# Optimization experiments

Measured on AMD Instinct MI355X. Metric: run time of the kernel, lower is better.

The kernel has to match this reference:

```python
import jax, jax.numpy as jnp
import numpy as np

T = 262144          # total packed neighbor tokens
D_IN, D_H, D_OUT = 128, 256, 128
N_SETS = 8192


def setup_inputs() -> dict:
    key = jax.random.key(0)
    k1, k2, k3, k4, k5, k6 = jax.random.split(key, 6)
    x = jax.random.normal(k1, (T, D_IN), dtype=jnp.float32)
    segment_ids = jnp.sort(jax.random.randint(k2, (T,), 0, N_SETS))
    # phi params (torch Linear: y = x @ W.T + b); store as [in, out] for einsum
    s1 = 1.0 / np.sqrt(D_IN)
    s2 = 1.0 / np.sqrt(D_H)
    W1 = jax.random.uniform(k3, (D_IN, D_H), jnp.float32, -s1, s1)
    b1 = jax.random.uniform(k4, (D_H,), jnp.float32, -s1, s1)
    W2 = jax.random.uniform(k5, (D_H, D_OUT), jnp.float32, -s2, s2)
    b2 = jax.random.uniform(k6, (D_OUT,), jnp.float32, -s2, s2)
    return {"x": x, "segment_ids": segment_ids, "num_segments": N_SETS,
            "W1": W1, "b1": b1, "W2": W2, "b2": b2}


def reference(x, segment_ids, num_segments, W1, b1, W2, b2):
    # phi: Linear -> ReLU -> Linear -> ReLU, applied to every packed token
    h = jax.nn.relu(x @ W1 + b1)            # [T, D_H]
    h = jax.nn.relu(h @ W2 + b2)            # [T, D_OUT]
    # per-set mean pool (segment mean over ragged sets)
    sums = jax.ops.segment_sum(h, segment_ids, num_segments=num_segments)  # [N, D_OUT]
    counts = jax.ops.segment_sum(jnp.ones((h.shape[0],), h.dtype), segment_ids,
                                 num_segments=num_segments)                 # [N]
    out = sums / jnp.maximum(counts, 1.0)[:, None]
    return out
```

## Files before the change

kernel.cpp:

```cpp
#include <hip/hip_runtime.h>

#define D_IN 128
#define D_H 256
#define D_OUT 128
#define N_SETS 8192
#define T_TOTAL 262144

typedef short short8 __attribute__((ext_vector_type(8)));
typedef float floatx4 __attribute__((ext_vector_type(4)));
typedef float floatx16 __attribute__((ext_vector_type(16)));
typedef unsigned int uint4v __attribute__((ext_vector_type(4)));

typedef const __attribute__((address_space(1))) unsigned int gu32;
typedef __attribute__((address_space(3))) unsigned int lu32;

union U8 { uint4v u; short8 s; };

__device__ inline unsigned short f32_bf16(float f) {
    unsigned int u = __float_as_uint(f);
    u += 0x7FFFu + ((u >> 16) & 1u);
    return (unsigned short)(u >> 16);
}

__global__ void setup_kernel(const float* __restrict__ W1, const float* __restrict__ W2,
                             unsigned short* __restrict__ W1s, unsigned short* __restrict__ W2s) {
    int t = blockIdx.x * 256 + threadIdx.x;
    int l = t & 63;
    int f = t >> 6;
    int hl = l >> 5, c31 = l & 31;
    if (f < 64) {
        int nt = f >> 3, c = f & 7;
        int k0 = c * 16 + hl * 8, n = nt * 32 + c31;
        unsigned short v[8];
#pragma unroll
        for (int j = 0; j < 8; j++) v[j] = f32_bf16(W1[(k0 + j) * D_H + n]);
#pragma unroll
        for (int j = 0; j < 8; j++) W1s[f * 512 + l * 8 + j] = v[j];
    } else {
        int g = f - 64;
        int o = g >> 4, c2 = g & 15;
        int k0 = c2 * 16 + hl * 8, n = o * 32 + c31;
        unsigned short v[8];
#pragma unroll
        for (int j = 0; j < 8; j++) v[j] = f32_bf16(W2[(k0 + j) * D_OUT + n]);
#pragma unroll
        for (int j = 0; j < 8; j++) W2s[g * 512 + l * 8 + j] = v[j];
    }
}

__global__ __launch_bounds__(768, 3) void ds_main(
    const float* __restrict__ x, const int* __restrict__ seg,
    const unsigned short* __restrict__ W1s, const float* __restrict__ b1,
    const unsigned short* __restrict__ W2s, const float* __restrict__ b2,
    float* __restrict__ out, float* __restrict__ counts)
{
    __shared__ __align__(16) unsigned short wbuf[128 * 512];
    __shared__ int ssegs[12][32];

    const int tid = threadIdx.x;
    const int wave = tid >> 6, lane = tid & 63;
    const int hl = lane >> 5, c31 = lane & 31;
    const int tok0 = blockIdx.x * 384 + wave * 32;
    const bool active = (tok0 < T_TOTAL);

    if (wave < 8) {
#pragma unroll
        for (int i = 0; i < 8; i++) {
            __builtin_amdgcn_global_load_lds((gu32*)(W1s + i * 4096 + tid * 8),
                                             (lu32*)(wbuf + i * 4096 + tid * 8), 16, 0, 0);
            __builtin_amdgcn_global_load_lds((gu32*)(W2s + i * 4096 + tid * 8),
                                             (lu32*)(wbuf + 32768 + i * 4096 + tid * 8), 16, 0, 0);
        }
    }

    int* sseg = ssegs[wave];

    short8 xfa[8];
    if (active) {
        if (lane < 32) sseg[lane] = seg[tok0 + lane];
        const float* xp = x + (size_t)(tok0 + c31) * D_IN + hl * 8;
#pragma unroll
        for (int c = 0; c < 8; c++) {
            float4 v0 = *(const float4*)(xp + c * 16);
            float4 v1 = *(const float4*)(xp + c * 16 + 4);
            unsigned int p0, p1, p2, p3;
            asm("v_cvt_pk_bf16_f32 %0, %1, %2" : "=v"(p0) : "v"(v0.x), "v"(v0.y));
            asm("v_cvt_pk_bf16_f32 %0, %1, %2" : "=v"(p1) : "v"(v0.z), "v"(v0.w));
            asm("v_cvt_pk_bf16_f32 %0, %1, %2" : "=v"(p2) : "v"(v1.x), "v"(v1.y));
            asm("v_cvt_pk_bf16_f32 %0, %1, %2" : "=v"(p3) : "v"(v1.z), "v"(v1.w));
            U8 u; u.u = (uint4v){p0, p1, p2, p3};
            xfa[c] = u.s;
        }
    }

    floatx16 acc2[4];
#pragma unroll
    for (int o = 0; o < 4; o++)
#pragma unroll
        for (int i = 0; i < 16; i++) acc2[o][i] = 0.f;

    __syncthreads();
    if (!active) return;

#pragma unroll
    for (int nt = 0; nt < 8; nt++) {
        floatx16 acc1;
#pragma unroll
        for (int i = 0; i < 16; i++) acc1[i] = 0.f;
#pragma unroll
        for (int c = 0; c < 8; c++) {
            short8 wf = *(const short8*)(wbuf + (nt * 8 + c) * 512 + lane * 8);
            acc1 = __builtin_amdgcn_mfma_f32_32x32x16_bf16(wf, xfa[c], acc1, 0, 0, 0);
        }
        float v[16];
#pragma unroll
        for (int g = 0; g < 4; g++) {
            floatx4 bv = *(const floatx4*)(b1 + nt * 32 + g * 8 + hl * 4);
#pragma unroll
            for (int i = 0; i < 4; i++) v[g * 4 + i] = fmaxf(acc1[g * 4 + i] + bv[i], 0.f);
        }
        unsigned int pk[8];
#pragma unroll
        for (int p = 0; p < 8; p++)
            asm("v_cvt_pk_bf16_f32 %0, %1, %2" : "=v"(pk[p]) : "v"(v[2 * p]), "v"(v[2 * p + 1]));
#pragma unroll
        for (int s = 0; s < 2; s++) {
            unsigned int d0 = pk[s * 4 + 0], d2 = pk[s * 4 + 2];
            asm("v_permlane32_swap_b32 %0, %1" : "+v"(d0), "+v"(d2));
            unsigned int d1 = pk[s * 4 + 1], d3 = pk[s * 4 + 3];
            asm("v_permlane32_swap_b32 %0, %1" : "+v"(d1), "+v"(d3));
            U8 u; u.u = (uint4v){d0, d1, d2, d3};
            const short8 hf = u.s;
            const int c2 = nt * 2 + s;
#pragma unroll
            for (int o = 0; o < 4; o++) {
                short8 bw = *(const short8*)(wbuf + (64 + o * 16 + c2) * 512 + lane * 8);
                acc2[o] = __builtin_amdgcn_mfma_f32_32x32x16_bf16(hf, bw, acc2[o], 0, 0, 0);
            }
        }
    }

    if (lane < 32) {
        int s = sseg[lane];
        if (lane == 0 || sseg[lane - 1] != s) {
            int len = 1;
            for (int u = lane + 1; u < 32 && sseg[u] == s; ++u) ++len;
            atomicAdd(&counts[s], (float)len);
        }
    }

    int sid[16];
#pragma unroll
    for (int e = 0; e < 16; e++) sid[e] = sseg[hl * 16 + e];

#pragma unroll
    for (int o = 0; o < 4; o++) {
        const float bias = b2[o * 32 + c31];
        float val[16];
#pragma unroll
        for (int r = 0; r < 16; r++) val[r] = fmaxf(acc2[o][r] + bias, 0.f);
        float st[16];
#pragma unroll
        for (int i = 0; i < 4; i++) {
            float a = val[i], b = val[8 + i];
            asm("v_permlane32_swap_b32 %0, %1" : "+v"(a), "+v"(b));
            st[i] = a; st[4 + i] = b;
            float c = val[4 + i], d = val[12 + i];
            asm("v_permlane32_swap_b32 %0, %1" : "+v"(c), "+v"(d));
            st[8 + i] = c; st[12 + i] = d;
        }
        const int col = o * 32 + c31;
        float sum = st[0];
#pragma unroll
        for (int e = 1; e < 16; e++) {
            if (sid[e] != sid[e - 1]) {
                atomicAdd(&out[(size_t)sid[e - 1] * D_OUT + col], sum);
                sum = 0.f;
            }
            sum += st[e];
        }
        atomicAdd(&out[(size_t)sid[15] * D_OUT + col], sum);
    }
}

__global__ void div_kernel(float4* __restrict__ out4, const float* __restrict__ counts) {
    int i = blockIdx.x * 256 + threadIdx.x;
    float inv = 1.f / fmaxf(counts[i >> 5], 1.f);
    float4 v = out4[i];
    v.x *= inv; v.y *= inv; v.z *= inv; v.w *= inv;
    out4[i] = v;
}

extern "C" void kernel_launch(void* const* d_in, const int* in_sizes, int n_in,
                              void* d_out, int out_size, void* d_ws, size_t ws_size,
                              hipStream_t stream) {
    const float* x  = (const float*)d_in[0];
    const int* seg  = (const int*)d_in[1];
    const float* W1 = (const float*)d_in[3];
    const float* b1 = (const float*)d_in[4];
    const float* W2 = (const float*)d_in[5];
    const float* b2 = (const float*)d_in[6];
    float* out = (float*)d_out;

    float* counts       = (float*)d_ws;
    unsigned short* W1s = (unsigned short*)((char*)d_ws + 32768);
    unsigned short* W2s = (unsigned short*)((char*)d_ws + 32768 + 65536);

    hipMemsetAsync(out, 0, (size_t)N_SETS * D_OUT * sizeof(float), stream);
    hipMemsetAsync(counts, 0, (size_t)N_SETS * sizeof(float), stream);
    hipLaunchKernelGGL(setup_kernel, dim3(32), dim3(256), 0, stream,
                       W1, W2, W1s, W2s);
    hipLaunchKernelGGL(ds_main, dim3(683), dim3(768), 0, stream,
                       x, seg, W1s, b1, W2s, b2, out, counts);
    hipLaunchKernelGGL(div_kernel, dim3(1024), dim3(256), 0, stream,
                       (float4*)out, counts);
}
```

Measured before the change: 252.4 us.

## Coalesce x loads via LDS staging and compute segment counts with ballot

```diff
diff --git a/kernel.cpp b/kernel.cpp
--- a/kernel.cpp
+++ b/kernel.cpp
@@ -10,6 +10,7 @@
 typedef float floatx4 __attribute__((ext_vector_type(4)));
 typedef float floatx16 __attribute__((ext_vector_type(16)));
 typedef unsigned int uint4v __attribute__((ext_vector_type(4)));
+typedef unsigned int uint2v __attribute__((ext_vector_type(2)));
 
 typedef const __attribute__((address_space(1))) unsigned int gu32;
 typedef __attribute__((address_space(3))) unsigned int lu32;
@@ -55,6 +56,7 @@
     float* __restrict__ out, float* __restrict__ counts)
 {
     __shared__ __align__(16) unsigned short wbuf[128 * 512];
+    __shared__ __align__(16) unsigned short xstg[12][32][40];
     __shared__ int ssegs[12][32];
 
     const int tid = threadIdx.x;
@@ -74,22 +76,36 @@
     }
 
     int* sseg = ssegs[wave];
-
+    unsigned short* xs = &xstg[wave][0][0];
+
+    float4 xv[16];
     short8 xfa[8];
     if (active) {
         if (lane < 32) sseg[lane] = seg[tok0 + lane];
-        const float* xp = x + (size_t)(tok0 + c31) * D_IN + hl * 8;
-#pragma unroll
-        for (int c = 0; c < 8; c++) {
-            float4 v0 = *(const float4*)(xp + c * 16);
-            float4 v1 = *(const float4*)(xp + c * 16 + 4);
-            unsigned int p0, p1, p2, p3;
-            asm("v_cvt_pk_bf16_f32 %0, %1, %2" : "=v"(p0) : "v"(v0.x), "v"(v0.y));
-            asm("v_cvt_pk_bf16_f32 %0, %1, %2" : "=v"(p1) : "v"(v0.z), "v"(v0.w));
-            asm("v_cvt_pk_bf16_f32 %0, %1, %2" : "=v"(p2) : "v"(v1.x), "v"(v1.y));
-            asm("v_cvt_pk_bf16_f32 %0, %1, %2" : "=v"(p3) : "v"(v1.z), "v"(v1.w));
-            U8 u; u.u = (uint4v){p0, p1, p2, p3};
-            xfa[c] = u.s;
+        const int tsub = lane >> 3, csub = lane & 7;
+#pragma unroll
+        for (int c4 = 0; c4 < 4; c4++)
+#pragma unroll
+            for (int i = 0; i < 4; i++)
+                xv[c4 * 4 + i] = *(const float4*)(
+                    x + (size_t)(tok0 + i * 8 + tsub) * D_IN + c4 * 32 + csub * 4);
+
+#pragma unroll
+        for (int c4 = 0; c4 < 4; c4++) {
+#pragma unroll
+            for (int i = 0; i < 4; i++) {
+                float4 v = xv[c4 * 4 + i];
+                unsigned p0, p1;
+                asm("v_cvt_pk_bf16_f32 %0, %1, %2" : "=v"(p0) : "v"(v.x), "v"(v.y));
+                asm("v_cvt_pk_bf16_f32 %0, %1, %2" : "=v"(p1) : "v"(v.z), "v"(v.w));
+                uint2v w; w[0] = p0; w[1] = p1;
+                *(__attribute__((address_space(3))) uint2v*)
+                    ((__attribute__((address_space(3))) unsigned short*)(xs) +
+                     (i * 8 + tsub) * 40 + csub * 4) = w;
+            }
+#pragma unroll
+            for (int cc = 0; cc < 2; cc++)
+                xfa[c4 * 2 + cc] = *(const short8*)(xs + (lane & 31) * 40 + cc * 16 + hl * 8);
         }
     }
 
@@ -140,12 +156,15 @@
         }
     }
 
-    if (lane < 32) {
-        int s = sseg[lane];
-        if (lane == 0 || sseg[lane - 1] != s) {
-            int len = 1;
-            for (int u = lane + 1; u < 32 && sseg[u] == s; ++u) ++len;
-            atomicAdd(&counts[s], (float)len);
+    {
+        int s_l = (lane < 32) ? sseg[lane] : 0;
+        int s_p = (lane > 0 && lane < 32) ? sseg[lane - 1] : -1;
+        bool head = (lane < 32) && (lane == 0 || s_p != s_l);
+        unsigned long long bal = __ballot(head);
+        if (head) {
+            unsigned long long rest = bal >> (lane + 1);
+            int next = rest ? (lane + 1 + __builtin_ctzll(rest)) : 32;
+            atomicAdd(&counts[s_l], (float)(next - lane));
         }
     }
 
```

Result: faster. 245.5 us (-2.7%).
